# Kernel tuning notes

Measured on AMD Instinct MI355X. Metric: run time of the kernel, lower is better.

The kernel has to match this reference:

```python
import jax, jax.numpy as jnp
import numpy as np

# 256 graphs x 1024 nodes, 64 channels, 4.19M edges (avg degree 16)
B, N, C, E = 256, 1024, 64, 4194304
RATIO = 0.5
K = 512  # ceil(RATIO * N), fixed per-graph keep count


def setup_inputs() -> dict:
    key = jax.random.key(0)
    k1, k2, k3, k4, k5, k6 = jax.random.split(key, 6)
    x = jax.random.normal(k1, (B * N, C), jnp.float32)
    w = jax.random.normal(k2, (1, C), jnp.float32) / np.sqrt(C)  # score_layer.weight
    b = jnp.zeros((1,), jnp.float32)                              # score_layer.bias
    # edges sampled within each graph so filter_adj semantics are realistic
    g = jax.random.randint(k3, (E,), 0, B)
    src = jax.random.randint(k4, (E,), 0, N)
    dst = jax.random.randint(k5, (E,), 0, N)
    edge_index = jnp.stack([g * N + src, g * N + dst]).astype(jnp.int32)
    edge_attr = jax.random.normal(k6, (E,), jnp.float32)
    batch = jnp.repeat(jnp.arange(B, dtype=jnp.int32), N)  # nondecreasing graph ids
    return {"x": x, "w": w, "b": b, "edge_index": edge_index,
            "edge_attr": edge_attr, "batch": batch}


def reference(x, w, b, edge_index, edge_attr, batch):
    # scores = Linear(x).squeeze() / ||W||  (bias also divided, as in source)
    scores = (x @ w.T + b)[:, 0] / jnp.linalg.norm(w)  # [B*N]
    # per-graph ratio top-k (equal-size graphs -> dense [B, N] top_k, fixed K)
    _, top_idx = jax.lax.top_k(scores.reshape(B, N), K)          # [B, K] local ids
    perm = (top_idx + (jnp.arange(B) * N)[:, None]).reshape(-1)  # [B*K] global ids
    x_p = x[perm]          # gather surviving node features
    batch_p = batch[perm]
    # filter_adj: relabel kept nodes 0..B*K-1, drop edges touching removed nodes.
    # For jit-able static shapes we keep [2, E] and mask dropped edges to -1
    # instead of compacting (mask returned for downstream compaction).
    new_idx = jnp.full((B * N,), -1, jnp.int32).at[perm].set(
        jnp.arange(B * K, dtype=jnp.int32))
    r = new_idx[edge_index[0]]
    c = new_idx[edge_index[1]]
    mask = (r >= 0) & (c >= 0)
    ei = jnp.where(mask, jnp.stack([r, c]), -1)
    ea = jnp.where(mask, edge_attr, jnp.zeros((), edge_attr.dtype))
    return x_p, ei, ea, batch_p, scores, perm, mask
```

## Files before the change

kernel.cpp:

```cpp
#include <hip/hip_runtime.h>
#include <math.h>

#define BGRAPHS 256
#define NNODES  1024
#define CCH     64
#define NEDGE   4194304
#define KKEEP   512

typedef unsigned long long u64;
typedef unsigned int u32;

#define OFF_XP   0
#define OFF_EI0  8388608
#define OFF_EI1  (8388608 + NEDGE)
#define OFF_EA   16777216
#define OFF_BP   20971520
#define OFF_SC   21102592
#define OFF_PM   21364736
#define OFF_MSK  21495808

__global__ __launch_bounds__(1024) void topk_kernel(
    const float* __restrict__ x, const float* __restrict__ w,
    const float* __restrict__ bias, const int* __restrict__ batch,
    float* __restrict__ xp, float* __restrict__ bpo, float* __restrict__ sco,
    float* __restrict__ pmo, int* __restrict__ new_idx)
{
    __shared__ float s_w[CCH];
    __shared__ u64 s_key[NNODES];

    const int b = blockIdx.x;
    const int tid = threadIdx.x;

    if (tid < CCH) s_w[tid] = w[tid];
    __syncthreads();

    double n2 = 0.0;
    #pragma unroll
    for (int k = 0; k < CCH; ++k) { double v = (double)s_w[k]; n2 += v * v; }
    const float nrm = (float)sqrt(n2);
    const float bv = bias[0];

    const float4* x4 = (const float4*)x;
    const int node = b * NNODES + tid;
    double acc = 0.0;
    #pragma unroll
    for (int k = 0; k < 16; ++k) {
        float4 xv = x4[node * 16 + k];
        acc += (double)xv.x * (double)s_w[4 * k + 0];
        acc += (double)xv.y * (double)s_w[4 * k + 1];
        acc += (double)xv.z * (double)s_w[4 * k + 2];
        acc += (double)xv.w * (double)s_w[4 * k + 3];
    }
    const float score = ((float)acc + bv) / nrm;
    sco[node] = score;

    u32 u = __float_as_uint(score);
    u32 mu = u ^ (u32)(((int)u >> 31) | 0x80000000);
    u32 hi = ~mu;
    s_key[tid] = ((u64)hi << 32) | (u32)tid;

    for (int k = 2; k <= NNODES; k <<= 1) {
        for (int j = k >> 1; j > 0; j >>= 1) {
            __syncthreads();
            int ixj = tid ^ j;
            if (ixj > tid) {
                u64 a = s_key[tid], c = s_key[ixj];
                bool up = ((tid & k) == 0);
                if ((a > c) == up) { s_key[tid] = c; s_key[ixj] = a; }
            }
        }
    }
    __syncthreads();

    const int lidx = (int)(u32)s_key[tid];
    if (tid < KKEEP) {
        const int g = b * NNODES + lidx;
        pmo[b * KKEEP + tid] = (float)g;
        bpo[b * KKEEP + tid] = (float)batch[g];
        new_idx[g] = b * KKEEP + tid;
    } else {
        new_idx[b * NNODES + lidx] = -1;
    }

    float4* xp4 = (float4*)xp;
    #pragma unroll
    for (int p = 0; p < 8; ++p) {
        int elem = tid + p * 1024;
        int row = elem >> 4, col = elem & 15;
        int src = (int)(u32)s_key[row];
        xp4[(b * KKEEP + row) * 16 + col] = x4[(b * NNODES + src) * 16 + col];
    }
}

__global__ __launch_bounds__(256) void edge_kernel(
    const int* __restrict__ ei, const float* __restrict__ ea,
    const int* __restrict__ new_idx,
    float* __restrict__ ei0o, float* __restrict__ ei1o,
    float* __restrict__ eao, float* __restrict__ msk)
{
    const int gid = blockIdx.x * 256 + threadIdx.x;
    const int4* s4p = (const int4*)ei;
    const int4* d4p = (const int4*)(ei + NEDGE);
    const float4* a4p = (const float4*)ea;

    int4 s4 = s4p[gid];
    int4 d4 = d4p[gid];
    float4 a4 = a4p[gid];
    float4 r4, c4, o4, m4;

#define PROC(comp)                                            \
    {                                                         \
        int r = new_idx[s4.comp];                             \
        int c = new_idx[d4.comp];                             \
        int m = (r >= 0) && (c >= 0);                         \
        r4.comp = m ? (float)r : -1.0f;                       \
        c4.comp = m ? (float)c : -1.0f;                       \
        o4.comp = m ? a4.comp : 0.0f;                         \
        m4.comp = (float)m;                                   \
    }
    PROC(x) PROC(y) PROC(z) PROC(w)
#undef PROC

    ((float4*)ei0o)[gid] = r4;
    ((float4*)ei1o)[gid] = c4;
    ((float4*)eao)[gid]  = o4;
    ((float4*)msk)[gid]  = m4;
}

extern "C" void kernel_launch(void* const* d_in, const int* in_sizes, int n_in,
                              void* d_out, int out_size, void* d_ws, size_t ws_size,
                              hipStream_t stream) {
    const float* x          = (const float*)d_in[0];
    const float* w          = (const float*)d_in[1];
    const float* bias       = (const float*)d_in[2];
    const int*   edge_index = (const int*)d_in[3];
    const float* edge_attr  = (const float*)d_in[4];
    const int*   batch      = (const int*)d_in[5];

    float* out = (float*)d_out;
    float* xp   = out + OFF_XP;
    float* ei0o = out + OFF_EI0;
    float* ei1o = out + OFF_EI1;
    float* eao  = out + OFF_EA;
    float* bpo  = out + OFF_BP;
    float* sco  = out + OFF_SC;
    float* pmo  = out + OFF_PM;
    float* msk  = out + OFF_MSK;

    int* new_idx = (int*)d_ws;

    topk_kernel<<<BGRAPHS, 1024, 0, stream>>>(x, w, bias, batch, xp, bpo, sco, pmo, new_idx);
    edge_kernel<<<NEDGE / 4 / 256, 256, 0, stream>>>(edge_index, edge_attr, new_idx,
                                                     ei0o, ei1o, eao, msk);
}
```

Measured before the change: 269.2 us.

## Split top-k into score/sort/gather kernels, compress relabel table to u16, nontemporal edge I/O

Splits the fused per-graph kernel into a wide score kernel, a 1024-thread bitonic sort kernel, and a separate fully parallel feature-gather kernel. The node relabel table shrinks from int32 to uint16 local indices, with the global new index rebuilt arithmetically from the graph id, halving the random-lookup footprint so it fits better in cache. Edge streams use nontemporal loads and stores to avoid polluting cache. This costs two extra launches and re-reading x and the scores between kernels.

New measurement: 251.6 us. -6.5%, faster.

```diff
diff --git a/kernel.cpp b/kernel.cpp
--- a/kernel.cpp
+++ b/kernel.cpp
@@ -9,6 +9,9 @@
 
 typedef unsigned long long u64;
 typedef unsigned int u32;
+typedef unsigned short u16;
+typedef float  f32x4 __attribute__((ext_vector_type(4)));
+typedef int    i32x4 __attribute__((ext_vector_type(4)));
 
 #define OFF_XP   0
 #define OFF_EI0  8388608
@@ -19,18 +22,12 @@
 #define OFF_PM   21364736
 #define OFF_MSK  21495808
 
-__global__ __launch_bounds__(1024) void topk_kernel(
+__global__ __launch_bounds__(256) void score_kernel(
     const float* __restrict__ x, const float* __restrict__ w,
-    const float* __restrict__ bias, const int* __restrict__ batch,
-    float* __restrict__ xp, float* __restrict__ bpo, float* __restrict__ sco,
-    float* __restrict__ pmo, int* __restrict__ new_idx)
+    const float* __restrict__ bias, float* __restrict__ sco)
 {
     __shared__ float s_w[CCH];
-    __shared__ u64 s_key[NNODES];
-
-    const int b = blockIdx.x;
     const int tid = threadIdx.x;
-
     if (tid < CCH) s_w[tid] = w[tid];
     __syncthreads();
 
@@ -40,24 +37,34 @@
     const float nrm = (float)sqrt(n2);
     const float bv = bias[0];
 
-    const float4* x4 = (const float4*)x;
-    const int node = b * NNODES + tid;
+    const int node = blockIdx.x * 256 + tid;
+    const f32x4* x4 = (const f32x4*)x;
     double acc = 0.0;
     #pragma unroll
     for (int k = 0; k < 16; ++k) {
-        float4 xv = x4[node * 16 + k];
+        f32x4 xv = x4[node * 16 + k];
         acc += (double)xv.x * (double)s_w[4 * k + 0];
         acc += (double)xv.y * (double)s_w[4 * k + 1];
         acc += (double)xv.z * (double)s_w[4 * k + 2];
         acc += (double)xv.w * (double)s_w[4 * k + 3];
     }
-    const float score = ((float)acc + bv) / nrm;
-    sco[node] = score;
+    sco[node] = ((float)acc + bv) / nrm;
+}
 
+__global__ __launch_bounds__(1024) void sort_kernel(
+    const float* __restrict__ sco, const int* __restrict__ batch,
+    float* __restrict__ pmo, float* __restrict__ bpo,
+    u16* __restrict__ table16, u16* __restrict__ src16)
+{
+    __shared__ u64 s_key[NNODES];
+    const int b = blockIdx.x;
+    const int tid = threadIdx.x;
+    const int node = b * NNODES + tid;
+
+    const float score = sco[node];
     u32 u = __float_as_uint(score);
     u32 mu = u ^ (u32)(((int)u >> 31) | 0x80000000);
-    u32 hi = ~mu;
-    s_key[tid] = ((u64)hi << 32) | (u32)tid;
+    s_key[tid] = ((u64)(~mu) << 32) | (u32)tid;
 
     for (int k = 2; k <= NNODES; k <<= 1) {
         for (int j = k >> 1; j > 0; j >>= 1) {
@@ -73,58 +80,65 @@
     __syncthreads();
 
     const int lidx = (int)(u32)s_key[tid];
+    const int g = b * NNODES + lidx;
     if (tid < KKEEP) {
-        const int g = b * NNODES + lidx;
         pmo[b * KKEEP + tid] = (float)g;
         bpo[b * KKEEP + tid] = (float)batch[g];
-        new_idx[g] = b * KKEEP + tid;
+        table16[g] = (u16)tid;
+        src16[b * KKEEP + tid] = (u16)lidx;
     } else {
-        new_idx[b * NNODES + lidx] = -1;
+        table16[g] = 0xFFFFu;
     }
+}
 
-    float4* xp4 = (float4*)xp;
-    #pragma unroll
-    for (int p = 0; p < 8; ++p) {
-        int elem = tid + p * 1024;
-        int row = elem >> 4, col = elem & 15;
-        int src = (int)(u32)s_key[row];
-        xp4[(b * KKEEP + row) * 16 + col] = x4[(b * NNODES + src) * 16 + col];
-    }
+__global__ __launch_bounds__(256) void gather_kernel(
+    const float* __restrict__ x, const u16* __restrict__ src16,
+    float* __restrict__ xp)
+{
+    const int elem = blockIdx.x * 256 + threadIdx.x;
+    const int row = elem >> 4;
+    const int col = elem & 15;
+    const int b = row >> 9;
+    const int src = (int)src16[row];
+    const f32x4* x4 = (const f32x4*)x;
+    ((f32x4*)xp)[elem] = x4[((b << 10) + src) * 16 + col];
 }
 
 __global__ __launch_bounds__(256) void edge_kernel(
     const int* __restrict__ ei, const float* __restrict__ ea,
-    const int* __restrict__ new_idx,
+    const u16* __restrict__ table16,
     float* __restrict__ ei0o, float* __restrict__ ei1o,
     float* __restrict__ eao, float* __restrict__ msk)
 {
     const int gid = blockIdx.x * 256 + threadIdx.x;
-    const int4* s4p = (const int4*)ei;
-    const int4* d4p = (const int4*)(ei + NEDGE);
-    const float4* a4p = (const float4*)ea;
+    const i32x4* s4p = (const i32x4*)ei;
+    const i32x4* d4p = (const i32x4*)(ei + NEDGE);
+    const f32x4* a4p = (const f32x4*)ea;
 
-    int4 s4 = s4p[gid];
-    int4 d4 = d4p[gid];
-    float4 a4 = a4p[gid];
-    float4 r4, c4, o4, m4;
+    i32x4 s4 = __builtin_nontemporal_load(&s4p[gid]);
+    i32x4 d4 = __builtin_nontemporal_load(&d4p[gid]);
+    f32x4 a4 = __builtin_nontemporal_load(&a4p[gid]);
+    f32x4 r4, c4, o4, m4;
 
-#define PROC(comp)                                            \
-    {                                                         \
-        int r = new_idx[s4.comp];                             \
-        int c = new_idx[d4.comp];                             \
-        int m = (r >= 0) && (c >= 0);                         \
-        r4.comp = m ? (float)r : -1.0f;                       \
-        c4.comp = m ? (float)c : -1.0f;                       \
-        o4.comp = m ? a4.comp : 0.0f;                         \
-        m4.comp = (float)m;                                   \
+#define PROC(comp)                                                 \
+    {                                                              \
+        u16 vs = table16[s4.comp];                                 \
+        u16 vd = table16[d4.comp];                                 \
+        int m = (vs != 0xFFFFu) && (vd != 0xFFFFu);                \
+        int r = ((s4.comp >> 10) << 9) + (int)vs;                  \
+        int c = ((d4.comp >> 10) << 9) + (int)vd;                  \
+        r4.comp = m ? (float)r : -1.0f;                            \
+        c4.comp = m ? (float)c : -1.0f;                            \
+        o4.comp = m ? a4.comp : 0.0f;                              \
+        m4.comp = (float)m;                                        \
     }
     PROC(x) PROC(y) PROC(z) PROC(w)
 #undef PROC
 
-    ((float4*)ei0o)[gid] = r4;
-    ((float4*)ei1o)[gid] = c4;
-    ((float4*)eao)[gid]  = o4;
-    ((float4*)msk)[gid]  = m4;
+    __builtin_nontemporal_store(r4, &((f32x4*)ei0o)[gid]);
+    __builtin_nontemporal_store(c4, &((f32x4*)ei1o)[gid]);
+    __builtin_nontemporal_store(o4, &((f32x4*)eao)[gid]);
+    __builtin_nontemporal_store(m4, &((f32x4*)msk)[gid]);
 }
 
 extern "C" void kernel_launch(void* const* d_in, const int* in_sizes, int n_in,
@@ -147,9 +161,12 @@
     float* pmo  = out + OFF_PM;
     float* msk  = out + OFF_MSK;
 
-    int* new_idx = (int*)d_ws;
+    u16* table16 = (u16*)d_ws;
+    u16* src16   = (u16*)d_ws + BGRAPHS * NNODES;
 
-    topk_kernel<<<BGRAPHS, 1024, 0, stream>>>(x, w, bias, batch, xp, bpo, sco, pmo, new_idx);
-    edge_kernel<<<NEDGE / 4 / 256, 256, 0, stream>>>(edge_index, edge_attr, new_idx,
+    score_kernel<<<BGRAPHS * NNODES / 256, 256, 0, stream>>>(x, w, bias, sco);
+    sort_kernel<<<BGRAPHS, 1024, 0, stream>>>(sco, batch, pmo, bpo, table16, src16);
+    gather_kernel<<<BGRAPHS * KKEEP * 16 / 256, 256, 0, stream>>>(x, src16, xp);
+    edge_kernel<<<NEDGE / 4 / 256, 256, 0, stream>>>(edge_index, edge_attr, table16,
                                                      ei0o, ei1o, eao, msk);
 }
```
